# Kernel tuning notes

Measured on AMD Instinct MI355X. Metric: run time of the kernel, lower is better.

## Reference

```python
import jax, jax.numpy as jnp
import numpy as np

N_ITERATION = 3
NEG_INF = -1e18
EPS = 1e-8


def squash(t, eps=EPS):
    # t: [..., E]; scale = |t|^2/(1+|t|^2), out = scale * t / |t|
    sq = jnp.sum(t * t, axis=-1, keepdims=True)
    return (sq / (1.0 + sq)) * t / (jnp.sqrt(sq) + eps)


def setup_inputs() -> dict:
    key = jax.random.key(0)
    k1, k2, k3, k4 = jax.random.split(key, 4)
    B, K, L, D, O, E = 8, 1024, 1024, 1024, 6, 128
    inputs_u = jax.random.normal(k1, (B, K, D), dtype=jnp.float32)
    context_sequence = jax.random.normal(k2, (B, L, D), dtype=jnp.float32)
    # route_weights: [num_out_caps, d_model, d_per_capsule], fan-in scaled
    route_weights = jax.random.normal(k3, (O, D, E), dtype=jnp.float32) / np.sqrt(D)
    # True = padded in-capsule (masked)
    inputs_mask = jax.random.randint(k4, (B, K), 0, 2).astype(bool)
    return {
        "inputs_u": inputs_u,
        "context_sequence": context_sequence,
        "route_weights": route_weights,
        "inputs_mask": inputs_mask,
    }


def reference(inputs_u, context_sequence, route_weights, inputs_mask):
    # priors_u_hat: [B, K, O, E] (shared route weights across in-capsules)
    priors = jnp.einsum("bkd,ode->bkoe", inputs_u, route_weights)
    B, K, O, E = priors.shape
    L = context_sequence.shape[1]
    logits = jnp.zeros((B, L, K, O), dtype=priors.dtype)
    mask4 = inputs_mask[:, None, :, None]  # [B,1,K,1] -> broadcast to [B,L,K,O]
    outputs_v = None
    probs_c = None
    for i in range(N_ITERATION):
        lg = jnp.where(mask4, NEG_INF, logits)
        probs_c = jax.nn.softmax(lg, axis=-1)  # softmax over out-capsules
        # weighted aggregation over in-capsules then squash: [B,L,O,E]
        outputs_v = squash(jnp.einsum("blko,bkoe->bloe", probs_c, priors))
        if i != N_ITERATION - 1:
            # agreement delta logits: [B,L,K,O]
            logits = logits + jnp.einsum("bkoe,bloe->blko", priors, outputs_v)
    return outputs_v, probs_c
```

## Files before the change

### kernel.cpp

```cpp
#include <hip/hip_runtime.h>
#include <hip/hip_bf16.h>
#include <stdint.h>

typedef __bf16 bf16_t;
typedef __bf16 bf16x8 __attribute__((ext_vector_type(8)));
typedef float f32x4 __attribute__((ext_vector_type(4)));

#define BB 8
#define KK 1024
#define LL 1024
#define DD 1024
#define OO 6
#define EE 128
#define NN 768

__device__ __forceinline__ void async_copy16(const void* gptr, void* lds) {
    __builtin_amdgcn_global_load_lds(
        (__attribute__((address_space(1))) void*)gptr,
        (__attribute__((address_space(3))) void*)lds,
        16, 0, 0);
}

__device__ __forceinline__ void split_bf16(float x, bf16_t& hi, bf16_t& lo) {
    hi = (bf16_t)x;
    lo = (bf16_t)(x - (float)hi);
}

__device__ __forceinline__ void squash_regs(const float* sp, float* vv, int lane) {
#pragma unroll
    for (int o = 0; o < 6; ++o) {
        float t = sp[2*o]*sp[2*o] + sp[2*o+1]*sp[2*o+1];
#pragma unroll
        for (int off = 32; off > 0; off >>= 1) t += __shfl_xor(t, off, 64);
        const float sc = t / (1.0f + t) / (sqrtf(t) + 1e-8f);
        vv[2*o]   = sc * sp[2*o];
        vv[2*o+1] = sc * sp[2*o+1];
    }
}

__global__ __launch_bounds__(256) void prep_kernel(
    const float* __restrict__ A, bf16_t* __restrict__ Ah, bf16_t* __restrict__ Al,
    const float* __restrict__ W, bf16_t* __restrict__ Wth, bf16_t* __restrict__ Wtl,
    float* __restrict__ sbuf)
{
    const int bx = blockIdx.x;
    if (bx < 8192) {
        const long i = ((long)bx * 256 + threadIdx.x) * 4;
        const float4 x = *(const float4*)(A + i);
        union { bf16_t h[4]; uint2 u; } ph, pl;
        split_bf16(x.x, ph.h[0], pl.h[0]);
        split_bf16(x.y, ph.h[1], pl.h[1]);
        split_bf16(x.z, ph.h[2], pl.h[2]);
        split_bf16(x.w, ph.h[3], pl.h[3]);
        *(uint2*)(Ah + i) = ph.u;
        *(uint2*)(Al + i) = pl.u;
    } else if (bx < 8960) {
        __shared__ float t[32][33];
        const int flat = bx - 8192;
        const int o  = flat / 128;
        const int rem = flat % 128;
        const int d0 = (rem & 31) * 32;
        const int e0 = (rem >> 5) * 32;
        const int tx = threadIdx.x & 31;
        const int ty = threadIdx.x >> 5;
        const float* Wo = W + (long)o * DD * EE;
        bf16_t* Ho = Wth + (long)o * EE * DD;
        bf16_t* Lo = Wtl + (long)o * EE * DD;
#pragma unroll
        for (int p = 0; p < 4; ++p)
            t[p * 8 + ty][tx] = Wo[(long)(d0 + p * 8 + ty) * EE + e0 + tx];
        __syncthreads();
#pragma unroll
        for (int p = 0; p < 4; ++p) {
            const float val = t[tx][p * 8 + ty];
            bf16_t h, l;
            split_bf16(val, h, l);
            const long idx = (long)(e0 + p * 8 + ty) * DD + d0 + tx;
            Ho[idx] = h;
            Lo[idx] = l;
        }
    } else {
        const int i = (bx - 8960) * 1024 + threadIdx.x;
#pragma unroll
        for (int r = 0; r < 4; ++r) {
            const int idx = (bx - 8960) * 1024 + r * 256 + threadIdx.x;
            if (idx < 3 * BB * NN) sbuf[idx] = 0.f;
        }
        (void)i;
    }
}

__global__ __launch_bounds__(256) void gemm_priors(
    const bf16_t* __restrict__ Ah, const bf16_t* __restrict__ Al,
    const bf16_t* __restrict__ Bh, const bf16_t* __restrict__ Bl,
    float* __restrict__ C, float* __restrict__ s0)
{
    __shared__ alignas(16) bf16_t sAh[128 * 32];
    __shared__ alignas(16) bf16_t sAl[128 * 32];
    __shared__ alignas(16) bf16_t sBh[64 * 32];
    __shared__ alignas(16) bf16_t sBl[64 * 32];
    __shared__ float sRed[64];

    const int bid  = blockIdx.x;
    const int xcd  = bid & 7;
    const int s    = bid >> 3;
    const int bn   = s % 12;
    const int bm   = (s / 12) * 8 + xcd;

    const int tid  = threadIdx.x;
    const int w    = tid >> 6;
    const int lane = tid & 63;
    const int qr   = (w >> 1) * 64;
    const int qc   = (w & 1) * 32;
    const int r16  = lane & 15;
    const int q    = lane >> 4;

    f32x4 acc[4][2] = {};

    const int mrowA = w * 32 + (lane >> 2);
    const int mrowB = w * 16 + (lane >> 2);
    const int kcol  = (lane & 3) * 8;

    const long aoff = (long)(bm * 128 + mrowA) * DD + kcol;
    const long boff = (long)(bn * 64  + mrowB) * DD + kcol;
    const bf16_t* gAh0 = Ah + aoff;  const bf16_t* gAh1 = gAh0 + 16 * DD;
    const bf16_t* gAl0 = Al + aoff;  const bf16_t* gAl1 = gAl0 + 16 * DD;
    const bf16_t* gBh  = Bh + boff;
    const bf16_t* gBl  = Bl + boff;

    bf16_t* lAh0 = sAh + (w * 2 + 0) * 512;
    bf16_t* lAh1 = sAh + (w * 2 + 1) * 512;
    bf16_t* lAl0 = sAl + (w * 2 + 0) * 512;
    bf16_t* lAl1 = sAl + (w * 2 + 1) * 512;
    bf16_t* lBh  = sBh + w * 512;
    bf16_t* lBl  = sBl + w * 512;

    for (int kt = 0; kt < DD / 32; ++kt) {
        const int k0 = kt * 32;
        async_copy16(gAh0 + k0, lAh0);
        async_copy16(gAh1 + k0, lAh1);
        async_copy16(gAl0 + k0, lAl0);
        async_copy16(gAl1 + k0, lAl1);
        async_copy16(gBh  + k0, lBh);
        async_copy16(gBl  + k0, lBl);
        __syncthreads();

        bf16x8 ah[4], al[4], bh[2], bl[2];
#pragma unroll
        for (int i = 0; i < 4; ++i) {
            const int ra = (qr + 16 * i + r16) * 32 + q * 8;
            ah[i] = *(const bf16x8*)(sAh + ra);
            al[i] = *(const bf16x8*)(sAl + ra);
        }
#pragma unroll
        for (int j = 0; j < 2; ++j) {
            const int rb = (qc + 16 * j + r16) * 32 + q * 8;
            bh[j] = *(const bf16x8*)(sBh + rb);
            bl[j] = *(const bf16x8*)(sBl + rb);
        }
#pragma unroll
        for (int i = 0; i < 4; ++i)
#pragma unroll
            for (int j = 0; j < 2; ++j) {
                acc[i][j] = __builtin_amdgcn_mfma_f32_16x16x32_bf16(
                    al[i], bh[j], acc[i][j], 0, 0, 0);
                acc[i][j] = __builtin_amdgcn_mfma_f32_16x16x32_bf16(
                    ah[i], bl[j], acc[i][j], 0, 0, 0);
                acc[i][j] = __builtin_amdgcn_mfma_f32_16x16x32_bf16(
                    ah[i], bh[j], acc[i][j], 0, 0, 0);
            }
        __syncthreads();
    }

#pragma unroll
    for (int i = 0; i < 4; ++i)
#pragma unroll
        for (int j = 0; j < 2; ++j) {
            const int col = bn * 64 + qc + 16 * j + r16;
#pragma unroll
            for (int r = 0; r < 4; ++r) {
                const int row = bm * 128 + qr + 16 * i + q * 4 + r;
                C[(long)row * NN + col] = acc[i][j][r];
            }
        }

    if (tid < 64) sRed[tid] = 0.f;
    __syncthreads();
#pragma unroll
    for (int j = 0; j < 2; ++j) {
        float cs = 0.f;
#pragma unroll
        for (int i = 0; i < 4; ++i)
            cs += acc[i][j][0] + acc[i][j][1] + acc[i][j][2] + acc[i][j][3];
        cs += __shfl_xor(cs, 16, 64);
        cs += __shfl_xor(cs, 32, 64);
        if (lane < 16)
            atomicAdd(&sRed[qc + 16 * j + r16], cs);
    }
    __syncthreads();
    if (tid < 64)
        atomicAdd(&s0[(bm >> 3) * NN + bn * 64 + tid], sRed[tid] * (1.0f / 6.0f));
}

__global__ __launch_bounds__(256) void pgs_kernel(
    const float* __restrict__ priors, const float* __restrict__ s_prev,
    const int* __restrict__ mask, float* __restrict__ g,
    float* __restrict__ probs, float* __restrict__ s_cur, int first)
{
    const int blk  = blockIdx.x;
    const int b    = blk >> 7;
    const int k8   = (blk & 127) * 8;
    const int w    = threadIdx.x >> 6;
    const int lane = threadIdx.x & 63;

    float vv[12];
    {
        float sp[12];
#pragma unroll
        for (int s = 0; s < 12; ++s) sp[s] = s_prev[b * NN + s * 64 + lane];
        squash_regs(sp, vv, lane);
    }

    float sacc[12];
#pragma unroll
    for (int s = 0; s < 12; ++s) sacc[s] = 0.f;

#pragma unroll
    for (int r = 0; r < 2; ++r) {
        const int k = k8 + w * 2 + r;
        const long rid = (long)b * KK + k;
        const float* pr = priors + rid * NN;
        float pp[12];
#pragma unroll
        for (int s = 0; s < 12; ++s) pp[s] = pr[s * 64 + lane];

        float d[6];
#pragma unroll
        for (int o = 0; o < 6; ++o) {
            float t = pp[2*o] * vv[2*o] + pp[2*o+1] * vv[2*o+1];
#pragma unroll
            for (int off = 32; off > 0; off >>= 1) t += __shfl_xor(t, off, 64);
            d[o] = t;
        }

        if (first) {
            if (lane < 6) {
                float x = d[0];
#pragma unroll
                for (int o = 1; o < 6; ++o) if (lane == o) x = d[o];
                g[rid * 6 + lane] = x;
            }
        } else {
#pragma unroll
            for (int o = 0; o < 6; ++o) d[o] += g[rid * 6 + o];
        }

        float p[6];
        if (mask[rid] != 0) {
#pragma unroll
            for (int o = 0; o < 6; ++o) p[o] = 1.0f / 6.0f;
        } else {
            float m = d[0];
#pragma unroll
            for (int o = 1; o < 6; ++o) m = fmaxf(m, d[o]);
            float ssum = 0.f;
#pragma unroll
            for (int o = 0; o < 6; ++o) { p[o] = expf(d[o] - m); ssum += p[o]; }
            const float inv = 1.0f / ssum;
#pragma unroll
            for (int o = 0; o < 6; ++o) p[o] *= inv;
        }

        if (!first && lane < 6) {
            float x = p[0];
#pragma unroll
            for (int o = 1; o < 6; ++o) if (lane == o) x = p[o];
            probs[rid * 6 + lane] = x;
        }

#pragma unroll
        for (int s = 0; s < 12; ++s) sacc[s] = fmaf(p[s >> 1], pp[s], sacc[s]);
    }

    __shared__ float red[4][768];
#pragma unroll
    for (int s = 0; s < 12; ++s) red[w][s * 64 + lane] = sacc[s];
    __syncthreads();
    const int t = threadIdx.x;
#pragma unroll
    for (int i = 0; i < 3; ++i) {
        const int flat = t + i * 256;
        atomicAdd(&s_cur[b * NN + flat],
                  red[0][flat] + red[1][flat] + red[2][flat] + red[3][flat]);
    }
}

__global__ __launch_bounds__(256) void bcast_kernel(
    const float* __restrict__ s2, const float* __restrict__ P,
    float* __restrict__ out)
{
    const int blk = blockIdx.x;
    if (blk < 2048) {
        const int b  = blk >> 8;
        const int l0 = (blk & 255) * 4;
        const int w = threadIdx.x >> 6, lane = threadIdx.x & 63;
        __shared__ float vrow[768];
        if (w == 0) {
            float sp[12], vv[12];
#pragma unroll
            for (int s = 0; s < 12; ++s) sp[s] = s2[b * NN + s * 64 + lane];
            squash_regs(sp, vv, lane);
#pragma unroll
            for (int s = 0; s < 12; ++s) vrow[s * 64 + lane] = vv[s];
        }
        __syncthreads();
        float* dst = out + ((long)b * LL + l0) * NN;
        const int t = threadIdx.x;
#pragma unroll
        for (int i = 0; i < 3; ++i) {
            const int idx = t * 12 + i * 4;
            *(float4*)(dst + idx) = *(const float4*)(vrow + (idx % NN));
        }
    } else {
        const long NVF = (long)BB * LL * OO * EE;
        const int blk2 = blk - 2048;
        const long base = (long)blk2 * 4096;
        const int b = (int)(base / ((long)LL * KK * OO));
        const int choff = (int)(base % (KK * OO));
        const float* src = P + (long)b * (KK * OO);
        float* dst = out + NVF + base;
        const int t = threadIdx.x;
#pragma unroll
        for (int i = 0; i < 4; ++i) {
            int off = choff + t * 16 + i * 4;
            if (off >= KK * OO) off -= KK * OO;
            *(float4*)(dst + t * 16 + i * 4) = *(const float4*)(src + off);
        }
    }
}

extern "C" void kernel_launch(void* const* d_in, const int* in_sizes, int n_in,
                              void* d_out, int out_size, void* d_ws, size_t ws_size,
                              hipStream_t stream)
{
    (void)in_sizes; (void)n_in; (void)out_size; (void)ws_size;
    const float* u    = (const float*)d_in[0];
    const float* W    = (const float*)d_in[2];
    const int*   mask = (const int*)d_in[3];
    float*       out  = (float*)d_out;

    char* ws = (char*)d_ws;
    size_t off = 0;
    float*  priors = (float*)(ws + off);  off += (size_t)8192 * NN * 4;
    bf16_t* Ah     = (bf16_t*)(ws + off); off += (size_t)8192 * DD * 2;
    bf16_t* Al     = (bf16_t*)(ws + off); off += (size_t)8192 * DD * 2;
    bf16_t* Wth    = (bf16_t*)(ws + off); off += (size_t)OO * EE * DD * 2;
    bf16_t* Wtl    = (bf16_t*)(ws + off); off += (size_t)OO * EE * DD * 2;
    float*  g      = (float*)(ws + off);  off += (size_t)BB * KK * OO * 4;
    float*  probs  = (float*)(ws + off);  off += (size_t)BB * KK * OO * 4;
    float*  sbuf   = (float*)(ws + off);  off += (size_t)3 * BB * NN * 4;
    float*  s0 = sbuf, *s1 = sbuf + BB * NN, *s2 = sbuf + 2 * BB * NN;

    hipLaunchKernelGGL(prep_kernel, dim3(8969), dim3(256), 0, stream,
                       u, Ah, Al, W, Wth, Wtl, sbuf);
    hipLaunchKernelGGL(gemm_priors, dim3(768), dim3(256), 0, stream,
                       Ah, Al, Wth, Wtl, priors, s0);
    hipLaunchKernelGGL(pgs_kernel, dim3(1024), dim3(256), 0, stream,
                       priors, s0, mask, g, probs, s1, 1);
    hipLaunchKernelGGL(pgs_kernel, dim3(1024), dim3(256), 0, stream,
                       priors, s1, mask, g, probs, s2, 0);
    hipLaunchKernelGGL(bcast_kernel, dim3(14336), dim3(256), 0, stream,
                       s2, probs, out);
}
```

Baseline: 373.7 us.

## Fuse probs broadcast into final routing pass and use 32x32 MFMA tiles

The second routing kernel now stages its softmax probabilities in shared memory and writes the L-broadcast probs output directly. This removes the intermediate probs buffer and the separate broadcast pass over it, leaving a smaller kernel that only broadcasts the squashed outputs. The priors GEMM also switches from 16x16x32 to 32x32x16 bf16 MFMA instructions, which cuts LDS fragment loads per MFMA and changes the accumulator layout and epilogue indexing. In exchange, each pgs block now issues a large strided store burst for the broadcast, which may be less coalesced than the old dedicated broadcast kernel.

```diff
diff --git a/kernel.cpp b/kernel.cpp
--- a/kernel.cpp
+++ b/kernel.cpp
@@ -4,7 +4,7 @@
 
 typedef __bf16 bf16_t;
 typedef __bf16 bf16x8 __attribute__((ext_vector_type(8)));
-typedef float f32x4 __attribute__((ext_vector_type(4)));
+typedef float f32x16 __attribute__((ext_vector_type(16)));
 
 #define BB 8
 #define KK 1024
@@ -80,13 +80,11 @@
             Lo[idx] = l;
         }
     } else {
-        const int i = (bx - 8960) * 1024 + threadIdx.x;
 #pragma unroll
         for (int r = 0; r < 4; ++r) {
             const int idx = (bx - 8960) * 1024 + r * 256 + threadIdx.x;
             if (idx < 3 * BB * NN) sbuf[idx] = 0.f;
         }
-        (void)i;
     }
 }
 
@@ -103,19 +101,19 @@
 
     const int bid  = blockIdx.x;
     const int xcd  = bid & 7;
-    const int s    = bid >> 3;
-    const int bn   = s % 12;
-    const int bm   = (s / 12) * 8 + xcd;
+    const int sgp  = bid >> 3;
+    const int bn   = sgp % 12;
+    const int bm   = (sgp / 12) * 8 + xcd;
 
     const int tid  = threadIdx.x;
     const int w    = tid >> 6;
     const int lane = tid & 63;
     const int qr   = (w >> 1) * 64;
     const int qc   = (w & 1) * 32;
-    const int r16  = lane & 15;
-    const int q    = lane >> 4;
-
-    f32x4 acc[4][2] = {};
+    const int l31  = lane & 31;
+    const int lh   = lane >> 5;
+
+    f32x16 acc[2] = {};
 
     const int mrowA = w * 32 + (lane >> 2);
     const int mrowB = w * 16 + (lane >> 2);
@@ -145,58 +143,51 @@
         async_copy16(gBl  + k0, lBl);
         __syncthreads();
 
-        bf16x8 ah[4], al[4], bh[2], bl[2];
-#pragma unroll
-        for (int i = 0; i < 4; ++i) {
-            const int ra = (qr + 16 * i + r16) * 32 + q * 8;
-            ah[i] = *(const bf16x8*)(sAh + ra);
-            al[i] = *(const bf16x8*)(sAl + ra);
-        }
-#pragma unroll
-        for (int j = 0; j < 2; ++j) {
-            const int rb = (qc + 16 * j + r16) * 32 + q * 8;
-            bh[j] = *(const bf16x8*)(sBh + rb);
-            bl[j] = *(const bf16x8*)(sBl + rb);
-        }
-#pragma unroll
-        for (int i = 0; i < 4; ++i)
-#pragma unroll
-            for (int j = 0; j < 2; ++j) {
-                acc[i][j] = __builtin_amdgcn_mfma_f32_16x16x32_bf16(
-                    al[i], bh[j], acc[i][j], 0, 0, 0);
-                acc[i][j] = __builtin_amdgcn_mfma_f32_16x16x32_bf16(
-                    ah[i], bl[j], acc[i][j], 0, 0, 0);
-                acc[i][j] = __builtin_amdgcn_mfma_f32_16x16x32_bf16(
-                    ah[i], bh[j], acc[i][j], 0, 0, 0);
+#pragma unroll
+        for (int kh = 0; kh < 2; ++kh) {
+            const int kb = kh * 16 + lh * 8;
+            bf16x8 ahf[2], alf[2], bhf, blf;
+#pragma unroll
+            for (int i = 0; i < 2; ++i) {
+                const int ra = (qr + i * 32 + l31) * 32 + kb;
+                ahf[i] = *(const bf16x8*)(sAh + ra);
+                alf[i] = *(const bf16x8*)(sAl + ra);
             }
+            const int rb = (qc + l31) * 32 + kb;
+            bhf = *(const bf16x8*)(sBh + rb);
+            blf = *(const bf16x8*)(sBl + rb);
+#pragma unroll
+            for (int i = 0; i < 2; ++i) {
+                acc[i] = __builtin_amdgcn_mfma_f32_32x32x16_bf16(
+                    alf[i], bhf, acc[i], 0, 0, 0);
+                acc[i] = __builtin_amdgcn_mfma_f32_32x32x16_bf16(
+                    ahf[i], blf, acc[i], 0, 0, 0);
+                acc[i] = __builtin_amdgcn_mfma_f32_32x32x16_bf16(
+                    ahf[i], bhf, acc[i], 0, 0, 0);
+            }
+        }
         __syncthreads();
     }
 
-#pragma unroll
-    for (int i = 0; i < 4; ++i)
-#pragma unroll
-        for (int j = 0; j < 2; ++j) {
-            const int col = bn * 64 + qc + 16 * j + r16;
-#pragma unroll
-            for (int r = 0; r < 4; ++r) {
-                const int row = bm * 128 + qr + 16 * i + q * 4 + r;
-                C[(long)row * NN + col] = acc[i][j][r];
-            }
-        }
+    const int col = bn * 64 + qc + l31;
+#pragma unroll
+    for (int i = 0; i < 2; ++i) {
+#pragma unroll
+        for (int r = 0; r < 16; ++r) {
+            const int row = bm * 128 + qr + i * 32 + (r & 3) + 8 * (r >> 2) + 4 * lh;
+            C[(long)row * NN + col] = acc[i][r];
+        }
+    }
 
     if (tid < 64) sRed[tid] = 0.f;
     __syncthreads();
-#pragma unroll
-    for (int j = 0; j < 2; ++j) {
-        float cs = 0.f;
-#pragma unroll
-        for (int i = 0; i < 4; ++i)
-            cs += acc[i][j][0] + acc[i][j][1] + acc[i][j][2] + acc[i][j][3];
-        cs += __shfl_xor(cs, 16, 64);
-        cs += __shfl_xor(cs, 32, 64);
-        if (lane < 16)
-            atomicAdd(&sRed[qc + 16 * j + r16], cs);
-    }
+    float cs = 0.f;
+#pragma unroll
+    for (int i = 0; i < 2; ++i)
+#pragma unroll
+        for (int r = 0; r < 16; ++r) cs += acc[i][r];
+    cs += __shfl_xor(cs, 32, 64);
+    if (lane < 32) atomicAdd(&sRed[qc + l31], cs);
     __syncthreads();
     if (tid < 64)
         atomicAdd(&s0[(bm >> 3) * NN + bn * 64 + tid], sRed[tid] * (1.0f / 6.0f));
@@ -205,7 +196,7 @@
 __global__ __launch_bounds__(256) void pgs_kernel(
     const float* __restrict__ priors, const float* __restrict__ s_prev,
     const int* __restrict__ mask, float* __restrict__ g,
-    float* __restrict__ probs, float* __restrict__ s_cur, int first)
+    float* __restrict__ s_cur, float* __restrict__ outP, int first)
 {
     const int blk  = blockIdx.x;
     const int b    = blk >> 7;
@@ -213,6 +204,9 @@
     const int w    = threadIdx.x >> 6;
     const int lane = threadIdx.x & 63;
 
+    __shared__ float red[4][768];
+    __shared__ float pstage[48];
+
     float vv[12];
     {
         float sp[12];
@@ -271,18 +265,17 @@
             for (int o = 0; o < 6; ++o) p[o] *= inv;
         }
 
-        if (!first && lane < 6) {
+        if (outP && lane < 6) {
             float x = p[0];
 #pragma unroll
             for (int o = 1; o < 6; ++o) if (lane == o) x = p[o];
-            probs[rid * 6 + lane] = x;
+            pstage[(w * 2 + r) * 6 + lane] = x;
         }
 
 #pragma unroll
         for (int s = 0; s < 12; ++s) sacc[s] = fmaf(p[s >> 1], pp[s], sacc[s]);
     }
 
-    __shared__ float red[4][768];
 #pragma unroll
     for (int s = 0; s < 12; ++s) red[w][s * 64 + lane] = sacc[s];
     __syncthreads();
@@ -293,49 +286,47 @@
         atomicAdd(&s_cur[b * NN + flat],
                   red[0][flat] + red[1][flat] + red[2][flat] + red[3][flat]);
     }
-}
-
-__global__ __launch_bounds__(256) void bcast_kernel(
-    const float* __restrict__ s2, const float* __restrict__ P,
-    float* __restrict__ out)
+
+    if (outP) {
+        float* base = outP + (long)b * (LL * KK * OO) + k8 * 6;
+        const int j = t & 3;
+        const int lsub = t >> 2;
+        const float4 c0 = *(const float4*)(pstage + j * 12);
+        const float4 c1 = *(const float4*)(pstage + j * 12 + 4);
+        const float4 c2 = *(const float4*)(pstage + j * 12 + 8);
+#pragma unroll
+        for (int lg = 0; lg < 16; ++lg) {
+            float* dst = base + (long)(lg * 64 + lsub) * (KK * OO) + j * 12;
+            *(float4*)(dst)     = c0;
+            *(float4*)(dst + 4) = c1;
+            *(float4*)(dst + 8) = c2;
+        }
+    }
+}
+
+__global__ __launch_bounds__(256) void bcast_v_kernel(
+    const float* __restrict__ s2, float* __restrict__ out)
 {
     const int blk = blockIdx.x;
-    if (blk < 2048) {
-        const int b  = blk >> 8;
-        const int l0 = (blk & 255) * 4;
-        const int w = threadIdx.x >> 6, lane = threadIdx.x & 63;
-        __shared__ float vrow[768];
-        if (w == 0) {
-            float sp[12], vv[12];
-#pragma unroll
-            for (int s = 0; s < 12; ++s) sp[s] = s2[b * NN + s * 64 + lane];
-            squash_regs(sp, vv, lane);
-#pragma unroll
-            for (int s = 0; s < 12; ++s) vrow[s * 64 + lane] = vv[s];
-        }
-        __syncthreads();
-        float* dst = out + ((long)b * LL + l0) * NN;
-        const int t = threadIdx.x;
-#pragma unroll
-        for (int i = 0; i < 3; ++i) {
-            const int idx = t * 12 + i * 4;
-            *(float4*)(dst + idx) = *(const float4*)(vrow + (idx % NN));
-        }
-    } else {
-        const long NVF = (long)BB * LL * OO * EE;
-        const int blk2 = blk - 2048;
-        const long base = (long)blk2 * 4096;
-        const int b = (int)(base / ((long)LL * KK * OO));
-        const int choff = (int)(base % (KK * OO));
-        const float* src = P + (long)b * (KK * OO);
-        float* dst = out + NVF + base;
-        const int t = threadIdx.x;
-#pragma unroll
-        for (int i = 0; i < 4; ++i) {
-            int off = choff + t * 16 + i * 4;
-            if (off >= KK * OO) off -= KK * OO;
-            *(float4*)(dst + t * 16 + i * 4) = *(const float4*)(src + off);
-        }
+    const int b  = blk >> 8;
+    const int l0 = (blk & 255) * 4;
+    const int w = threadIdx.x >> 6, lane = threadIdx.x & 63;
+    __shared__ float vrow[768];
+    if (w == 0) {
+        float sp[12], vvv[12];
+#pragma unroll
+        for (int s = 0; s < 12; ++s) sp[s] = s2[b * NN + s * 64 + lane];
+        squash_regs(sp, vvv, lane);
+#pragma unroll
+        for (int s = 0; s < 12; ++s) vrow[s * 64 + lane] = vvv[s];
+    }
+    __syncthreads();
+    float* dst = out + ((long)b * LL + l0) * NN;
+    const int t = threadIdx.x;
+#pragma unroll
+    for (int i = 0; i < 3; ++i) {
+        const int idx = t * 12 + i * 4;
+        *(float4*)(dst + idx) = *(const float4*)(vrow + (idx % NN));
     }
 }
 
@@ -357,18 +348,19 @@
     bf16_t* Wth    = (bf16_t*)(ws + off); off += (size_t)OO * EE * DD * 2;
     bf16_t* Wtl    = (bf16_t*)(ws + off); off += (size_t)OO * EE * DD * 2;
     float*  g      = (float*)(ws + off);  off += (size_t)BB * KK * OO * 4;
-    float*  probs  = (float*)(ws + off);  off += (size_t)BB * KK * OO * 4;
     float*  sbuf   = (float*)(ws + off);  off += (size_t)3 * BB * NN * 4;
     float*  s0 = sbuf, *s1 = sbuf + BB * NN, *s2 = sbuf + 2 * BB * NN;
+
+    const long NVF = (long)BB * LL * OO * EE;
 
     hipLaunchKernelGGL(prep_kernel, dim3(8969), dim3(256), 0, stream,
                        u, Ah, Al, W, Wth, Wtl, sbuf);
     hipLaunchKernelGGL(gemm_priors, dim3(768), dim3(256), 0, stream,
                        Ah, Al, Wth, Wtl, priors, s0);
     hipLaunchKernelGGL(pgs_kernel, dim3(1024), dim3(256), 0, stream,
-                       priors, s0, mask, g, probs, s1, 1);
+                       priors, s0, mask, g, s1, (float*)nullptr, 1);
     hipLaunchKernelGGL(pgs_kernel, dim3(1024), dim3(256), 0, stream,
-                       priors, s1, mask, g, probs, s2, 0);
-    hipLaunchKernelGGL(bcast_kernel, dim3(14336), dim3(256), 0, stream,
-                       s2, probs, out);
-}
+                       priors, s1, mask, g, s2, out + NVF, 0);
+    hipLaunchKernelGGL(bcast_v_kernel, dim3(2048), dim3(256), 0, stream,
+                       s2, out);
+}
```

New measurement: 366.8 us (median of 2 runs). About the same (-1.9%).
